# Optimization experiments

Measured on AMD Instinct MI355X. Metric: run time of the kernel, lower is better.

Reference implementation:

```python
import jax, jax.numpy as jnp
import numpy as np

# Dimensions: B sequences, T max length, K tagset size
B, T, K = 512, 512, 128
START_TAG_IDX, END_TAG_IDX = 126, 127
NEG = -10000.0  # matches torch.full(..., -10000)


def setup_inputs() -> dict:
    key = jax.random.key(0)
    k1, k2, k3 = jax.random.split(key, 3)
    feats = jax.random.normal(k1, (B, T, K), dtype=jnp.float32)
    trans = jax.random.normal(k2, (K, K), dtype=jnp.float32)
    # __init__ clamps illegal transitions: into START, out of END
    trans = trans.at[:, START_TAG_IDX].set(NEG)
    trans = trans.at[END_TAG_IDX, :].set(NEG)
    # pack_sequence requires length-descending order; lengths in [1, T]
    lengths = jnp.sort(jax.random.randint(k3, (B,), 1, T + 1))[::-1].astype(jnp.int32)
    return {"feats": feats, "trans": trans, "lengths": lengths}


def reference(feats, trans, lengths):
    # CRF log-partition (score_z): forward algorithm over a padded batch.
    # Equivalent to the packed-sequence loop: at step t only sequences with
    # t < length update alpha; others keep their previous alpha.
    Bq, Tq, Kq = feats.shape
    alpha0 = jnp.full((Bq, Kq), NEG, dtype=feats.dtype).at[:, START_TAG_IDX].set(0.0)
    feats_t = jnp.swapaxes(feats, 0, 1)                       # [T,B,K]
    mask = jnp.arange(Tq, dtype=lengths.dtype)[:, None] < lengths[None, :]  # [T,B]

    def step(alpha, inp):
        f, m = inp  # f: [B,K] emissions, m: [B] legal mask
        # score[b,i,j] = feat[b,j] + alpha[b,i] + trans[i,j]
        score = f[:, None, :] + alpha[:, :, None] + trans[None, :, :]  # [B,K,K]
        alpha_new = jax.nn.logsumexp(score, axis=1)                    # [B,K]
        return jnp.where(m[:, None], alpha_new, alpha), None

    alpha, _ = jax.lax.scan(step, alpha0, (feats_t, mask))
    final = alpha + trans[:, END_TAG_IDX][None, :]
    return jnp.sum(jax.nn.logsumexp(final, axis=1))
```

## Files before the change

kernel.cpp:

```cpp
#include <hip/hip_runtime.h>

#define K_TAGS 128
#define T_MAX  512
#define N_SEQ  512
#define START_TAG 126
#define END_TAG   127
#define LOG2E 1.44269504088896340736f
#define LN2   0.69314718055994530942f

typedef float v2f __attribute__((ext_vector_type(2)));

__device__ __forceinline__ float fexp2(float x) {
#if __has_builtin(__builtin_amdgcn_exp2f)
  return __builtin_amdgcn_exp2f(x);
#else
  return exp2f(x);
#endif
}
__device__ __forceinline__ float flog2(float x) {
#if __has_builtin(__builtin_amdgcn_logf)
  return __builtin_amdgcn_logf(x);
#else
  return __log2f(x);
#endif
}

template <int CTRL>
__device__ __forceinline__ float dpp_mov(float x) {
  return __int_as_float(__builtin_amdgcn_update_dpp(
      0, __float_as_int(x), CTRL, 0xF, 0xF, true));
}

__device__ __forceinline__ void lds_barrier() {
  asm volatile("s_waitcnt lgkmcnt(0)" ::: "memory");
  __builtin_amdgcn_s_barrier();
  asm volatile("" ::: "memory");
}

__global__ __launch_bounds__(256, 2) void crf_fwd_kernel(
    const float* __restrict__ feats,
    const float* __restrict__ trans,
    const int*   __restrict__ lengths,
    float*       __restrict__ partial)
{
  const int blk = blockIdx.x;
  const int b   = (blk < N_SEQ / 2) ? blk : (3 * N_SEQ / 2 - 1 - blk);
  const int tid = (int)threadIdx.x;
  const int jg  = tid >> 2;
  const int q   = tid & 3;
  const int j0  = jg;
  const int j1  = jg + 64;
  const int i0  = q * 32;

  const int len = lengths[b];
  const float* fb = feats + (size_t)b * (T_MAX * K_TAGS);

  __shared__ __align__(16) float p_sh[2][K_TAGS];
  __shared__ __align__(16) float red16[16];
  __shared__ float red8[8];

  v2f E0[16], E1[16];
#pragma unroll
  for (int c = 0; c < 8; ++c) {
    const int r = i0 + 4 * (c ^ (q << 1));
    E0[2 * c + 0] = v2f{fexp2(trans[(r + 0) * K_TAGS + j0] * LOG2E),
                        fexp2(trans[(r + 1) * K_TAGS + j0] * LOG2E)};
    E0[2 * c + 1] = v2f{fexp2(trans[(r + 2) * K_TAGS + j0] * LOG2E),
                        fexp2(trans[(r + 3) * K_TAGS + j0] * LOG2E)};
    E1[2 * c + 0] = v2f{fexp2(trans[(r + 0) * K_TAGS + j1] * LOG2E),
                        fexp2(trans[(r + 1) * K_TAGS + j1] * LOG2E)};
    E1[2 * c + 1] = v2f{fexp2(trans[(r + 2) * K_TAGS + j1] * LOG2E),
                        fexp2(trans[(r + 3) * K_TAGS + j1] * LOG2E)};
  }

  if (q == 0) {
    p_sh[0][j0] = (j0 == START_TAG) ? 1.0f : 0.0f;
    p_sh[0][j1] = (j1 == START_TAG) ? 1.0f : 0.0f;
  }

  float Cc  = 0.0f;
  float pc0 = 0.0f, pc1 = 0.0f;

  float fA0, fA1, fB0, fB1, fC0, fC1, fD0, fD1;
  {
    const int tB = (len > 1) ? 1 : 0;
    const int tC = (len > 2) ? 2 : (len - 1);
    const int tD = (len > 3) ? 3 : (len - 1);
    fA0 = fb[j0];                fA1 = fb[j1];
    fB0 = fb[tB * K_TAGS + j0];  fB1 = fb[tB * K_TAGS + j1];
    fC0 = fb[tC * K_TAGS + j0];  fC1 = fb[tC * K_TAGS + j1];
    fD0 = fb[tD * K_TAGS + j0];  fD1 = fb[tD * K_TAGS + j1];
  }

#define BODY(BUF, F0, F1, ODD, TT)                                           \
  {                                                                          \
    const float fl0 = F0, fl1 = F1;      \
    const int tp = ((TT) + 4 < len) ? ((TT) + 4) : (len - 1);                \
    F0 = fb[tp * K_TAGS + j0];    \
    F1 = fb[tp * K_TAGS + j1];                                               \
    lds_barrier();                                                           \
    float D = 0.0f;                                                          \
    if (ODD) {     \
      const float4 r0 = *reinterpret_cast<const float4*>(&red16[0]);         \
      const float4 r1 = *reinterpret_cast<const float4*>(&red16[4]);         \
      const float4 r2 = *reinterpret_cast<const float4*>(&red16[8]);         \
      const float4 r3 = *reinterpret_cast<const float4*>(&red16[12]);        \
      float mm = fmaxf(fmaxf(fmaxf(r0.x, r0.y), fmaxf(r0.z, r0.w)),          \
                       fmaxf(fmaxf(r1.x, r1.y), fmaxf(r1.z, r1.w)));         \
      mm = fmaxf(mm, fmaxf(fmaxf(fmaxf(r2.x, r2.y), fmaxf(r2.z, r2.w)),     \
                           fmaxf(fmaxf(r3.x, r3.y), fmaxf(r3.z, r3.w))));   \
      D = flog2(mm);                                                         \
      Cc += D;                                                               \
    }                                                                        \
    const float* pp = p_sh[BUF];                                             \
    v2f s0a = {0.f, 0.f}, s0b = {0.f, 0.f};                                  \
    v2f s1a = {0.f, 0.f}, s1b = {0.f, 0.f};                                  \
    _Pragma("unroll")                                                        \
    for (int c = 0; c < 8; ++c) {                                            \
      const int w0 = i0 + 4 * (c ^ (q << 1));                                \
      const float4 pv = *reinterpret_cast<const float4*>(pp + w0);           \
      const v2f pA = {pv.x, pv.y};                                           \
      const v2f pB = {pv.z, pv.w};                                           \
      s0a = __builtin_elementwise_fma(pA, E0[2 * c + 0], s0a);               \
      s0b = __builtin_elementwise_fma(pB, E0[2 * c + 1], s0b);               \
      s1a = __builtin_elementwise_fma(pA, E1[2 * c + 0], s1a);               \
      s1b = __builtin_elementwise_fma(pB, E1[2 * c + 1], s1b);               \
    }                                                                        \
    const v2f s0 = s0a + s0b;                                                \
    const v2f s1 = s1a + s1b;                                                \
    float acc0 = s0.x + s0.y;                                                \
    float acc1 = s1.x + s1.y;                                                \
    acc0 += dpp_mov<0xB1>(acc0);                                             \
    acc0 += dpp_mov<0x4E>(acc0);                                             \
    acc1 += dpp_mov<0xB1>(acc1);                                             \
    acc1 += dpp_mov<0x4E>(acc1);                                             \
    const float g0 = fexp2(fmaf(fl0, LOG2E, -D));     \
    const float g1 = fexp2(fmaf(fl1, LOG2E, -D));                            \
    pc0 = acc0 * g0;                                                         \
    pc1 = acc1 * g1;                                                         \
    if (q < 2) p_sh[(BUF) ^ 1][(q == 0) ? j0 : j1] = (q == 0) ? pc0 : pc1;   \
    if (!(ODD)) {      \
      float mx = fmaxf(pc0, pc1);                                            \
      mx = fmaxf(mx, dpp_mov<0x124>(mx));                                    \
      mx = fmaxf(mx, dpp_mov<0x128>(mx));                                    \
      if ((tid & 15) == 0) red16[tid >> 4] = mx;                             \
    }                                                                        \
  }

  int t = 0;
  for (; t + 4 <= len; t += 4) {
    BODY(0, fA0, fA1, 0, t)
    BODY(1, fB0, fB1, 1, t + 1)
    BODY(0, fC0, fC1, 0, t + 2)
    BODY(1, fD0, fD1, 1, t + 3)
  }
  const int rem = len - t;
  if (rem > 0) BODY(0, fA0, fA1, 0, t)
  if (rem > 1) BODY(1, fB0, fB1, 1, t + 1)
  if (rem > 2) BODY(0, fC0, fC1, 0, t + 2)
#undef BODY

  const float fin0 = flog2(pc0) + Cc + trans[j0 * K_TAGS + END_TAG] * LOG2E;
  const float fin1 = flog2(pc1) + Cc + trans[j1 * K_TAGS + END_TAG] * LOG2E;

  float m = fmaxf(fin0, fin1);
#pragma unroll
  for (int off = 4; off < 64; off <<= 1)
    m = fmaxf(m, __shfl_xor(m, off, 64));
  if ((tid & 63) == 0) red8[tid >> 6] = m;
  __syncthreads();
  const float Mf = fmaxf(fmaxf(red8[0], red8[1]), fmaxf(red8[2], red8[3]));

  float e = (q == 0) ? (fexp2(fin0 - Mf) + fexp2(fin1 - Mf)) : 0.0f;
#pragma unroll
  for (int off = 1; off < 64; off <<= 1)
    e += __shfl_xor(e, off, 64);
  if ((tid & 63) == 0) red8[4 + (tid >> 6)] = e;
  __syncthreads();
  if (tid == 0) {
    const float s = (red8[4] + red8[5]) + (red8[6] + red8[7]);
    partial[b] = (Mf + flog2(s)) * LN2;
  }
}

__global__ void crf_reduce(const float* __restrict__ partial,
                           float* __restrict__ out) {
  const int tid = (int)threadIdx.x;
  float s = partial[tid] + partial[tid + 256];
#pragma unroll
  for (int off = 1; off < 64; off <<= 1) s += __shfl_xor(s, off, 64);
  __shared__ float ws[4];
  if ((tid & 63) == 0) ws[tid >> 6] = s;
  __syncthreads();
  if (tid == 0) out[0] = (ws[0] + ws[1]) + (ws[2] + ws[3]);
}

extern "C" void kernel_launch(void* const* d_in, const int* in_sizes, int n_in,
                              void* d_out, int out_size, void* d_ws, size_t ws_size,
                              hipStream_t stream) {
  const float* feats   = (const float*)d_in[0];
  const float* trans   = (const float*)d_in[1];
  const int*   lengths = (const int*)d_in[2];
  float* partial = (float*)d_ws;
  float* out     = (float*)d_out;

  crf_fwd_kernel<<<dim3(N_SEQ), dim3(256), 0, stream>>>(feats, trans, lengths, partial);
  crf_reduce<<<dim3(1), dim3(256), 0, stream>>>(partial, out);
}
```

Baseline: 324.8 us.

## Split reduction dimension across 8 lanes, each lane owning 4 output tags

Each thread now handles 4 output columns over a 16-row slice of the reduction instead of 2 columns over 32 rows. The 8-lane reduction uses two DPP steps plus a ds_swizzle. The max-rescale bookkeeping moves to a double-buffered red16, computed on even steps and consumed two steps later. This is meant to cut per-step serial FMA chain length and per-step latency on the recurrence critical path, at the cost of more cross-lane reduction steps and more emission loads per thread.

```diff
diff --git a/kernel.cpp b/kernel.cpp
--- a/kernel.cpp
+++ b/kernel.cpp
@@ -29,6 +29,10 @@
 __device__ __forceinline__ float dpp_mov(float x) {
   return __int_as_float(__builtin_amdgcn_update_dpp(
       0, __float_as_int(x), CTRL, 0xF, 0xF, true));
+}
+template <int OFF>
+__device__ __forceinline__ float swz(float x) {
+  return __int_as_float(__builtin_amdgcn_ds_swizzle(__float_as_int(x), OFF));
 }
 
 __device__ __forceinline__ void lds_barrier() {
@@ -46,132 +50,152 @@
   const int blk = blockIdx.x;
   const int b   = (blk < N_SEQ / 2) ? blk : (3 * N_SEQ / 2 - 1 - blk);
   const int tid = (int)threadIdx.x;
-  const int jg  = tid >> 2;
-  const int q   = tid & 3;
-  const int j0  = jg;
-  const int j1  = jg + 64;
-  const int i0  = q * 32;
+  const int jg  = tid >> 3;
+  const int q   = tid & 7;
+  const int r0  = q * 16;
+  const int cs  = q >> 1;
 
   const int len = lengths[b];
   const float* fb = feats + (size_t)b * (T_MAX * K_TAGS);
 
   __shared__ __align__(16) float p_sh[2][K_TAGS];
-  __shared__ __align__(16) float red16[16];
+  __shared__ __align__(16) float red16[2][16];
   __shared__ float red8[8];
 
-  v2f E0[16], E1[16];
-#pragma unroll
-  for (int c = 0; c < 8; ++c) {
-    const int r = i0 + 4 * (c ^ (q << 1));
-    E0[2 * c + 0] = v2f{fexp2(trans[(r + 0) * K_TAGS + j0] * LOG2E),
-                        fexp2(trans[(r + 1) * K_TAGS + j0] * LOG2E)};
-    E0[2 * c + 1] = v2f{fexp2(trans[(r + 2) * K_TAGS + j0] * LOG2E),
-                        fexp2(trans[(r + 3) * K_TAGS + j0] * LOG2E)};
-    E1[2 * c + 0] = v2f{fexp2(trans[(r + 0) * K_TAGS + j1] * LOG2E),
-                        fexp2(trans[(r + 1) * K_TAGS + j1] * LOG2E)};
-    E1[2 * c + 1] = v2f{fexp2(trans[(r + 2) * K_TAGS + j1] * LOG2E),
-                        fexp2(trans[(r + 3) * K_TAGS + j1] * LOG2E)};
+  v2f E[4][8];
+#pragma unroll
+  for (int c = 0; c < 4; ++c) {
+    const int r = r0 + 4 * (c ^ cs);
+#pragma unroll
+    for (int k = 0; k < 4; ++k) {
+      const int col = jg + 32 * k;
+      E[k][2 * c + 0] = v2f{fexp2(trans[(r + 0) * K_TAGS + col] * LOG2E),
+                            fexp2(trans[(r + 1) * K_TAGS + col] * LOG2E)};
+      E[k][2 * c + 1] = v2f{fexp2(trans[(r + 2) * K_TAGS + col] * LOG2E),
+                            fexp2(trans[(r + 3) * K_TAGS + col] * LOG2E)};
+    }
   }
 
   if (q == 0) {
-    p_sh[0][j0] = (j0 == START_TAG) ? 1.0f : 0.0f;
-    p_sh[0][j1] = (j1 == START_TAG) ? 1.0f : 0.0f;
-  }
-
-  float Cc  = 0.0f;
-  float pc0 = 0.0f, pc1 = 0.0f;
-
-  float fA0, fA1, fB0, fB1, fC0, fC1, fD0, fD1;
+#pragma unroll
+    for (int k = 0; k < 4; ++k)
+      p_sh[0][jg + 32 * k] = (jg + 32 * k == START_TAG) ? 1.0f : 0.0f;
+  }
+  if (tid < 32) red16[tid >> 4][tid & 15] = 1.0f;
+
+  float Cc = 0.0f;
+  float pc0 = 0.f, pc1 = 0.f, pc2 = 0.f, pc3 = 0.f;
+
+  float4 FA, FB, FC, FD;
   {
     const int tB = (len > 1) ? 1 : 0;
     const int tC = (len > 2) ? 2 : (len - 1);
     const int tD = (len > 3) ? 3 : (len - 1);
-    fA0 = fb[j0];                fA1 = fb[j1];
-    fB0 = fb[tB * K_TAGS + j0];  fB1 = fb[tB * K_TAGS + j1];
-    fC0 = fb[tC * K_TAGS + j0];  fC1 = fb[tC * K_TAGS + j1];
-    fD0 = fb[tD * K_TAGS + j0];  fD1 = fb[tD * K_TAGS + j1];
-  }
-
-#define BODY(BUF, F0, F1, ODD, TT)                                           \
+    const float* a = fb + jg;
+    FA = float4{a[0], a[32], a[64], a[96]};
+    a = fb + tB * K_TAGS + jg;
+    FB = float4{a[0], a[32], a[64], a[96]};
+    a = fb + tC * K_TAGS + jg;
+    FC = float4{a[0], a[32], a[64], a[96]};
+    a = fb + tD * K_TAGS + jg;
+    FD = float4{a[0], a[32], a[64], a[96]};
+  }
+
+#define BODY(BUF, F, EVEN, SLOT, TT)                                         \
   {                                                                          \
-    const float fl0 = F0, fl1 = F1;      \
+    const float4 fl = F;             \
     const int tp = ((TT) + 4 < len) ? ((TT) + 4) : (len - 1);                \
-    F0 = fb[tp * K_TAGS + j0];    \
-    F1 = fb[tp * K_TAGS + j1];                                               \
+    const float* fr = fb + tp * K_TAGS + jg;                                 \
+    F.x = fr[0]; F.y = fr[32]; F.z = fr[64]; F.w = fr[96];                   \
     lds_barrier();                                                           \
     float D = 0.0f;                                                          \
-    if (ODD) {     \
-      const float4 r0 = *reinterpret_cast<const float4*>(&red16[0]);         \
-      const float4 r1 = *reinterpret_cast<const float4*>(&red16[4]);         \
-      const float4 r2 = *reinterpret_cast<const float4*>(&red16[8]);         \
-      const float4 r3 = *reinterpret_cast<const float4*>(&red16[12]);        \
-      float mm = fmaxf(fmaxf(fmaxf(r0.x, r0.y), fmaxf(r0.z, r0.w)),          \
-                       fmaxf(fmaxf(r1.x, r1.y), fmaxf(r1.z, r1.w)));         \
-      mm = fmaxf(mm, fmaxf(fmaxf(fmaxf(r2.x, r2.y), fmaxf(r2.z, r2.w)),     \
-                           fmaxf(fmaxf(r3.x, r3.y), fmaxf(r3.z, r3.w))));   \
+    if (EVEN) {                          \
+      const float4 m0 = *reinterpret_cast<const float4*>(&red16[(SLOT)^1][0]);  \
+      const float4 m1 = *reinterpret_cast<const float4*>(&red16[(SLOT)^1][4]);  \
+      const float4 m2 = *reinterpret_cast<const float4*>(&red16[(SLOT)^1][8]);  \
+      const float4 m3 = *reinterpret_cast<const float4*>(&red16[(SLOT)^1][12]); \
+      float mm = fmaxf(fmaxf(fmaxf(m0.x, m0.y), fmaxf(m0.z, m0.w)),          \
+                       fmaxf(fmaxf(m1.x, m1.y), fmaxf(m1.z, m1.w)));         \
+      mm = fmaxf(mm, fmaxf(fmaxf(fmaxf(m2.x, m2.y), fmaxf(m2.z, m2.w)),     \
+                           fmaxf(fmaxf(m3.x, m3.y), fmaxf(m3.z, m3.w))));   \
       D = flog2(mm);                                                         \
       Cc += D;                                                               \
     }                                                                        \
     const float* pp = p_sh[BUF];                                             \
-    v2f s0a = {0.f, 0.f}, s0b = {0.f, 0.f};                                  \
-    v2f s1a = {0.f, 0.f}, s1b = {0.f, 0.f};                                  \
+    v2f sA0 = {0.f,0.f}, sA1 = {0.f,0.f}, sA2 = {0.f,0.f}, sA3 = {0.f,0.f};  \
+    v2f sB0 = {0.f,0.f}, sB1 = {0.f,0.f}, sB2 = {0.f,0.f}, sB3 = {0.f,0.f};  \
     _Pragma("unroll")                                                        \
-    for (int c = 0; c < 8; ++c) {                                            \
-      const int w0 = i0 + 4 * (c ^ (q << 1));                                \
+    for (int c = 0; c < 4; ++c) {                                            \
+      const int w0 = r0 + 4 * (c ^ cs);                                      \
       const float4 pv = *reinterpret_cast<const float4*>(pp + w0);           \
       const v2f pA = {pv.x, pv.y};                                           \
       const v2f pB = {pv.z, pv.w};                                           \
-      s0a = __builtin_elementwise_fma(pA, E0[2 * c + 0], s0a);               \
-      s0b = __builtin_elementwise_fma(pB, E0[2 * c + 1], s0b);               \
-      s1a = __builtin_elementwise_fma(pA, E1[2 * c + 0], s1a);               \
-      s1b = __builtin_elementwise_fma(pB, E1[2 * c + 1], s1b);               \
-    }                                                                        \
-    const v2f s0 = s0a + s0b;                                                \
-    const v2f s1 = s1a + s1b;                                                \
-    float acc0 = s0.x + s0.y;                                                \
-    float acc1 = s1.x + s1.y;                                                \
-    acc0 += dpp_mov<0xB1>(acc0);                                             \
-    acc0 += dpp_mov<0x4E>(acc0);                                             \
-    acc1 += dpp_mov<0xB1>(acc1);                                             \
-    acc1 += dpp_mov<0x4E>(acc1);                                             \
-    const float g0 = fexp2(fmaf(fl0, LOG2E, -D));     \
-    const float g1 = fexp2(fmaf(fl1, LOG2E, -D));                            \
-    pc0 = acc0 * g0;                                                         \
-    pc1 = acc1 * g1;                                                         \
-    if (q < 2) p_sh[(BUF) ^ 1][(q == 0) ? j0 : j1] = (q == 0) ? pc0 : pc1;   \
-    if (!(ODD)) {      \
-      float mx = fmaxf(pc0, pc1);                                            \
-      mx = fmaxf(mx, dpp_mov<0x124>(mx));                                    \
-      mx = fmaxf(mx, dpp_mov<0x128>(mx));                                    \
-      if ((tid & 15) == 0) red16[tid >> 4] = mx;                             \
+      sA0 = __builtin_elementwise_fma(pA, E[0][2 * c + 0], sA0);             \
+      sB0 = __builtin_elementwise_fma(pB, E[0][2 * c + 1], sB0);             \
+      sA1 = __builtin_elementwise_fma(pA, E[1][2 * c + 0], sA1);             \
+      sB1 = __builtin_elementwise_fma(pB, E[1][2 * c + 1], sB1);             \
+      sA2 = __builtin_elementwise_fma(pA, E[2][2 * c + 0], sA2);             \
+      sB2 = __builtin_elementwise_fma(pB, E[2][2 * c + 1], sB2);             \
+      sA3 = __builtin_elementwise_fma(pA, E[3][2 * c + 0], sA3);             \
+      sB3 = __builtin_elementwise_fma(pB, E[3][2 * c + 1], sB3);             \
+    }                                                                        \
+    const v2f t0 = sA0 + sB0, t1 = sA1 + sB1, t2 = sA2 + sB2, t3 = sA3 + sB3;\
+    float a0 = t0.x + t0.y, a1 = t1.x + t1.y;                                \
+    float a2 = t2.x + t2.y, a3 = t3.x + t3.y;                                \
+    a0 += dpp_mov<0xB1>(a0); a1 += dpp_mov<0xB1>(a1);                        \
+    a2 += dpp_mov<0xB1>(a2); a3 += dpp_mov<0xB1>(a3);                        \
+    a0 += dpp_mov<0x4E>(a0); a1 += dpp_mov<0x4E>(a1);                        \
+    a2 += dpp_mov<0x4E>(a2); a3 += dpp_mov<0x4E>(a3);                        \
+    a0 += swz<0x101F>(a0); a1 += swz<0x101F>(a1);                            \
+    a2 += swz<0x101F>(a2); a3 += swz<0x101F>(a3);                            \
+    const float g0 = fexp2(fmaf(fl.x, LOG2E, -D));                           \
+    const float g1 = fexp2(fmaf(fl.y, LOG2E, -D));                           \
+    const float g2 = fexp2(fmaf(fl.z, LOG2E, -D));                           \
+    const float g3 = fexp2(fmaf(fl.w, LOG2E, -D));                           \
+    pc0 = a0 * g0; pc1 = a1 * g1; pc2 = a2 * g2; pc3 = a3 * g3;              \
+    if (q == 0) {                  \
+      float* pw = &p_sh[(BUF) ^ 1][jg];                                      \
+      pw[0] = pc0; pw[32] = pc1; pw[64] = pc2; pw[96] = pc3;                 \
+    }                                                                        \
+    if (EVEN) {                    \
+      float mx = fmaxf(fmaxf(pc0, pc1), fmaxf(pc2, pc3));                    \
+      mx = fmaxf(mx, swz<0x201F>(mx));                                       \
+      if ((tid & 15) == 0) red16[SLOT][tid >> 4] = mx;                       \
     }                                                                        \
   }
 
   int t = 0;
   for (; t + 4 <= len; t += 4) {
-    BODY(0, fA0, fA1, 0, t)
-    BODY(1, fB0, fB1, 1, t + 1)
-    BODY(0, fC0, fC1, 0, t + 2)
-    BODY(1, fD0, fD1, 1, t + 3)
+    BODY(0, FA, 1, 0, t)
+    BODY(1, FB, 0, 0, t + 1)
+    BODY(0, FC, 1, 1, t + 2)
+    BODY(1, FD, 0, 1, t + 3)
   }
   const int rem = len - t;
-  if (rem > 0) BODY(0, fA0, fA1, 0, t)
-  if (rem > 1) BODY(1, fB0, fB1, 1, t + 1)
-  if (rem > 2) BODY(0, fC0, fC1, 0, t + 2)
+  if (rem > 0) BODY(0, FA, 1, 0, t)
+  if (rem > 1) BODY(1, FB, 0, 0, t + 1)
+  if (rem > 2) BODY(0, FC, 1, 1, t + 2)
 #undef BODY
 
-  const float fin0 = flog2(pc0) + Cc + trans[j0 * K_TAGS + END_TAG] * LOG2E;
-  const float fin1 = flog2(pc1) + Cc + trans[j1 * K_TAGS + END_TAG] * LOG2E;
-
-  float m = fmaxf(fin0, fin1);
-#pragma unroll
-  for (int off = 4; off < 64; off <<= 1)
+  __syncthreads();
+
+  const float fin0 = flog2(pc0) + Cc + trans[(jg +  0) * K_TAGS + END_TAG] * LOG2E;
+  const float fin1 = flog2(pc1) + Cc + trans[(jg + 32) * K_TAGS + END_TAG] * LOG2E;
+  const float fin2 = flog2(pc2) + Cc + trans[(jg + 64) * K_TAGS + END_TAG] * LOG2E;
+  const float fin3 = flog2(pc3) + Cc + trans[(jg + 96) * K_TAGS + END_TAG] * LOG2E;
+
+  float m = fmaxf(fmaxf(fin0, fin1), fmaxf(fin2, fin3));
+#pragma unroll
+  for (int off = 8; off < 64; off <<= 1)
     m = fmaxf(m, __shfl_xor(m, off, 64));
   if ((tid & 63) == 0) red8[tid >> 6] = m;
   __syncthreads();
   const float Mf = fmaxf(fmaxf(red8[0], red8[1]), fmaxf(red8[2], red8[3]));
 
-  float e = (q == 0) ? (fexp2(fin0 - Mf) + fexp2(fin1 - Mf)) : 0.0f;
+  float e = 0.0f;
+  if (q == 0)
+    e = (fexp2(fin0 - Mf) + fexp2(fin1 - Mf)) +
+        (fexp2(fin2 - Mf) + fexp2(fin3 - Mf));
 #pragma unroll
   for (int off = 1; off < 64; off <<= 1)
     e += __shfl_xor(e, off, 64);
```

Result: slower. 395.4 us (+21.7%).
